# Kernel tuning notes

Hardware: AMD Instinct MI355X
Metric: run time of the kernel (lower is better)

## Reference

```python
import jax, jax.numpy as jnp
import numpy as np

B, Himg, Wimg, C, NH = 16, 64, 64, 256, 8
HD = C // NH  # 32
N = Himg * Wimg  # 4096


def _rotations(h, w, hd):
    # RMT/RAVLT 2D axial RoPE: head_dim split into two halves (rows, cols),
    # each half holds k_max = hd//4 complex frequencies.
    k_max = hd // 4
    theta = 1.0 / (10000.0 ** (np.arange(k_max) / k_max))
    ang_h = np.arange(h)[:, None] * theta  # (h, k_max)
    ang_w = np.arange(w)[:, None] * theta  # (w, k_max)
    ang = np.concatenate([
        np.broadcast_to(ang_h[:, None, :], (h, w, k_max)),
        np.broadcast_to(ang_w[None, :, :], (h, w, k_max)),
    ], axis=-1)  # (h, w, hd//2)
    return jnp.asarray(np.cos(ang), jnp.float32), jnp.asarray(np.sin(ang), jnp.float32)

COS, SIN = _rotations(Himg, Wimg, HD)


def _rope(x):
    # x: (b, nh, H, W, hd); complex rotation of (even, odd) channel pairs
    xr, xi = x[..., 0::2], x[..., 1::2]
    out_r = xr * COS - xi * SIN
    out_i = xr * SIN + xi * COS
    return jnp.stack([out_r, out_i], axis=-1).reshape(x.shape)


def setup_inputs() -> dict:
    key = jax.random.key(0)
    ks = jax.random.split(key, 5)
    return {
        "x": jax.random.normal(ks[0], (B, N, C), jnp.float32),
        "w_qkvo": jax.random.normal(ks[1], (C, 4 * C), jnp.float32) * 0.02,
        "b_qkvo": jnp.zeros((4 * C,), jnp.float32),
        "lepe_w": jax.random.normal(ks[2], (C, 1, 5, 5), jnp.float32) * 0.02,
        "lepe_b": jnp.zeros((C,), jnp.float32),
        "w_proj": jax.random.normal(ks[3], (C, C), jnp.float32) * 0.02,
        "b_proj": jnp.zeros((C,), jnp.float32),
    }


def reference(x, w_qkvo, b_qkvo, lepe_w, lepe_b, w_proj, b_proj):
    b, n, c = x.shape
    scale = HD ** -0.5
    qkvo = x @ w_qkvo + b_qkvo  # (b, n, 4c)
    q, k, v, o = (qkvo[..., i * c:(i + 1) * c] for i in range(4))
    # LePE: depthwise 5x5 conv on v viewed as an image
    v_img = v.reshape(b, Himg, Wimg, c).transpose(0, 3, 1, 2)  # NCHW
    lepe = jax.lax.conv_general_dilated(
        v_img, lepe_w, window_strides=(1, 1), padding=[(2, 2), (2, 2)],
        dimension_numbers=("NCHW", "OIHW", "NCHW"), feature_group_count=c,
    ) + lepe_b[None, :, None, None]
    # ELU+1 feature map
    q = jax.nn.elu(q) + 1.0
    k = jax.nn.elu(k) + 1.0
    q = q.reshape(b, n, NH, HD).transpose(0, 2, 1, 3)  # (b, nh, n, hd)
    k = k.reshape(b, n, NH, HD).transpose(0, 2, 1, 3)
    v = v.reshape(b, n, NH, HD).transpose(0, 2, 1, 3)
    # efficiency reweighting of keys
    q_mean = q.mean(axis=-2, keepdims=True)  # (b, nh, 1, hd)
    eff = jax.nn.softmax(scale * jnp.einsum("bhod,bhnd->bhon", q_mean, k), axis=-1)
    k = k * eff.transpose(0, 1, 3, 2) * n  # (b, nh, n, hd)
    # RoPE on q and reweighted k
    q_rope = _rope(q.reshape(b, NH, Himg, Wimg, HD)).reshape(b, NH, n, HD)
    k_rope = _rope(k.reshape(b, NH, Himg, Wimg, HD)).reshape(b, NH, n, HD)
    # normalizer from non-rope q and mean of reweighted k
    z = 1.0 / (jnp.einsum("bhnd,bhod->bhno", q, k.mean(axis=-2, keepdims=True)) + 1e-6)
    # linear attention: kv accumulation then q @ kv (scale n^-1 split as n^-0.5 each)
    inv_sqrt_n = n ** -0.5
    kv = jnp.einsum("bhnd,bhne->bhde", k_rope * inv_sqrt_n, v * inv_sqrt_n)  # (b, nh, hd, hd)
    out = jnp.einsum("bhnd,bhde->bhne", q_rope, kv) * z
    out = out.transpose(0, 2, 1, 3).reshape(b, n, c)
    out = out + lepe.transpose(0, 2, 3, 1).reshape(b, n, c)
    out = out * o  # gate
    return out @ w_proj + b_proj
```

## Files before the change

kernel.cpp:

```cpp
#include <hip/hip_runtime.h>
#include <math.h>

constexpr int B   = 16;
constexpr int IH  = 64;
constexpr int IW  = 64;
constexpr int C   = 256;
constexpr int NH  = 8;
constexpr int HD  = 32;
constexpr int N   = IH * IW;
constexpr int C4  = 4 * C;
constexpr int KVP_STRIDE = 1060;

using f16x8 = __attribute__((ext_vector_type(8))) _Float16;
using f32x4 = __attribute__((ext_vector_type(4))) float;

__global__ void k_tables(float* __restrict__ cosT, float* __restrict__ sinT) {
  int t = blockIdx.x * 256 + threadIdx.x;
  int j = t & 15, pix = t >> 4;
  int y = pix >> 6, x = pix & 63;
  int jj = j & 7;
  double theta = pow(10000.0, -(double)jj / 8.0);
  double pos = (j < 8) ? (double)y : (double)x;
  double ang = pos * theta;
  cosT[t] = (float)cos(ang);
  sinT[t] = (float)sin(ang);
}

__global__ void k_split_wT(const float* __restrict__ w, int ldb,
                           _Float16* __restrict__ hiT, _Float16* __restrict__ loT) {
  int n = blockIdx.x;
  int k = threadIdx.x;
  float v = w[(size_t)k * ldb + n];
  _Float16 h = (_Float16)v;
  hiT[(size_t)n * 256 + k] = h;
  loT[(size_t)n * 256 + k] = (_Float16)(v - (float)h);
}

__global__ __launch_bounds__(256) void k_gemm_split(
    const float* __restrict__ A, int lda,
    const _Float16* __restrict__ BhT, const _Float16* __restrict__ BlT,
    const float* __restrict__ bias, float* __restrict__ Cm, int ldc,
    int nelu, float* __restrict__ qpart) {
  __shared__ _Float16 lds[4 * 5120];
  _Float16* AhL = lds;
  _Float16* AlL = lds + 5120;
  _Float16* BhL = lds + 10240;
  _Float16* BlL = lds + 15360;
  int t = threadIdx.x;
  int m0 = blockIdx.x * 128, n0 = blockIdx.y * 128;
  int lane = t & 63;
  int wm = t >> 7, wn = (t >> 6) & 1;
  int lr = lane & 15, lg = lane >> 4;
  int srow = t >> 1, sseg = t & 1;

  f32x4 acc[4][4] = {};

  const float* aP = &A[(size_t)(m0 + srow) * lda + sseg * 16];
  const _Float16* bhP = &BhT[(size_t)(n0 + srow) * 256 + sseg * 16];
  const _Float16* blP = &BlT[(size_t)(n0 + srow) * 256 + sseg * 16];

  float4 areg[2][4];
#pragma unroll
  for (int j = 0; j < 4; ++j) areg[0][j] = *(const float4*)(aP + (j << 2));
#pragma unroll
  for (int j = 0; j < 4; ++j) areg[1][j] = *(const float4*)(aP + 32 + (j << 2));
  f16x8 brh0 = *(const f16x8*)(bhP + 0);
  f16x8 brh1 = *(const f16x8*)(bhP + 8);
  f16x8 brl0 = *(const f16x8*)(blP + 0);
  f16x8 brl1 = *(const f16x8*)(blP + 8);

#pragma unroll
  for (int it = 0; it < 8; ++it) {
    const int kc = it * 32;
    const int cur = it & 1;
    {
      float av[16];
#pragma unroll
      for (int j = 0; j < 4; ++j) {
        av[j * 4 + 0] = areg[cur][j].x; av[j * 4 + 1] = areg[cur][j].y;
        av[j * 4 + 2] = areg[cur][j].z; av[j * 4 + 3] = areg[cur][j].w;
      }
      f16x8 h0, h1, l0, l1;
#pragma unroll
      for (int j = 0; j < 8; ++j) {
        _Float16 h = (_Float16)av[j];
        h0[j] = h; l0[j] = (_Float16)(av[j] - (float)h);
        _Float16 h2 = (_Float16)av[j + 8];
        h1[j] = h2; l1[j] = (_Float16)(av[j + 8] - (float)h2);
      }
      int d = srow * 40 + sseg * 16;
      *(f16x8*)&AhL[d] = h0; *(f16x8*)&AhL[d + 8] = h1;
      *(f16x8*)&AlL[d] = l0; *(f16x8*)&AlL[d + 8] = l1;
      *(f16x8*)&BhL[d] = brh0; *(f16x8*)&BhL[d + 8] = brh1;
      *(f16x8*)&BlL[d] = brl0; *(f16x8*)&BlL[d + 8] = brl1;
    }
    __syncthreads();

    if (it < 6) {
#pragma unroll
      for (int j = 0; j < 4; ++j)
        areg[cur][j] = *(const float4*)(aP + kc + 64 + (j << 2));
    }
    if (it < 7) {
      brh0 = *(const f16x8*)(bhP + kc + 32);
      brh1 = *(const f16x8*)(bhP + kc + 40);
      brl0 = *(const f16x8*)(blP + kc + 32);
      brl1 = *(const f16x8*)(blP + kc + 40);
    }

    f16x8 ah[4], al[4];
#pragma unroll
    for (int mi = 0; mi < 4; ++mi) {
      int ar = (wm * 64 + mi * 16 + lr) * 40 + lg * 8;
      ah[mi] = *(const f16x8*)&AhL[ar];
      al[mi] = *(const f16x8*)&AlL[ar];
    }
#pragma unroll
    for (int ni = 0; ni < 4; ++ni) {
      int br = (wn * 64 + ni * 16 + lr) * 40 + lg * 8;
      f16x8 bh = *(const f16x8*)&BhL[br];
      f16x8 bl = *(const f16x8*)&BlL[br];
#pragma unroll
      for (int mi = 0; mi < 4; ++mi) {
        acc[mi][ni] = __builtin_amdgcn_mfma_f32_16x16x32_f16(ah[mi], bh, acc[mi][ni], 0, 0, 0);
        acc[mi][ni] = __builtin_amdgcn_mfma_f32_16x16x32_f16(al[mi], bh, acc[mi][ni], 0, 0, 0);
        acc[mi][ni] = __builtin_amdgcn_mfma_f32_16x16x32_f16(ah[mi], bl, acc[mi][ni], 0, 0, 0);
      }
    }
    __syncthreads();
  }

  float* Cl = reinterpret_cast<float*>(lds);
  int ri2 = t >> 3, c0 = (t & 7) << 4;
  bool doq = (qpart != nullptr) && (n0 < 256);
  float qs[16] = {};
#pragma unroll
  for (int mi = 0; mi < 4; ++mi) {
#pragma unroll
    for (int ni = 0; ni < 4; ++ni) {
      int col = wn * 64 + ni * 16 + lr;
#pragma unroll
      for (int r = 0; r < 4; ++r)
        Cl[(wm * 16 + lg * 4 + r) * 132 + col] = acc[mi][ni][r];
    }
    __syncthreads();
    int grow = m0 + (ri2 >> 4) * 64 + mi * 16 + (ri2 & 15);
#pragma unroll
    for (int j = 0; j < 4; ++j) {
      int col = n0 + c0 + j * 4;
      float4 v = *(const float4*)&Cl[ri2 * 132 + c0 + j * 4];
      float4 bb = *(const float4*)&bias[col];
      v.x += bb.x; v.y += bb.y; v.z += bb.z; v.w += bb.w;
      if (col < nelu) {
        v.x = (v.x > 0.f) ? v.x + 1.f : expf(v.x);
        v.y = (v.y > 0.f) ? v.y + 1.f : expf(v.y);
        v.z = (v.z > 0.f) ? v.z + 1.f : expf(v.z);
        v.w = (v.w > 0.f) ? v.w + 1.f : expf(v.w);
      }
      if (doq) {
        qs[j * 4 + 0] += v.x; qs[j * 4 + 1] += v.y;
        qs[j * 4 + 2] += v.z; qs[j * 4 + 3] += v.w;
      }
      *(float4*)&Cm[(size_t)grow * ldc + col] = v;
    }
    __syncthreads();
  }
  if (doq) {
#pragma unroll
    for (int j = 0; j < 4; ++j) {
      float4 w4 = {qs[j*4+0], qs[j*4+1], qs[j*4+2], qs[j*4+3]};
      *(float4*)&Cl[ri2 * 132 + c0 + j * 4] = w4;
    }
    __syncthreads();
    if (t < 128) {
      float ssum = 0.f;
#pragma unroll
      for (int rr = 0; rr < 32; ++rr) ssum += Cl[rr * 132 + t];
      int b_local = m0 >> 12, rowblk = (m0 >> 7) & 31;
      qpart[(size_t)(b_local * 32 + rowblk) * 256 + n0 + t] = ssum;
    }
  }
}

__global__ __launch_bounds__(256) void k_kvflash(
    const float* __restrict__ qkvo, const float* __restrict__ qpart,
    const float* __restrict__ cosT, const float* __restrict__ sinT,
    float* __restrict__ kvp) {
  __shared__ float qm[32];
  __shared__ float sL[512];
  __shared__ float red[256];
  __shared__ float ktG[4][32][36];
  __shared__ float vtG[4][32][36];
  int bh = blockIdx.x, chunk = blockIdx.y;
  int b = bh >> 3, h = bh & 7;
  int t = threadIdx.x;
  int nbase = chunk << 9;

  if (t < 32) {
    float s = 0.f;
#pragma unroll
    for (int rb = 0; rb < 32; ++rb)
      s += qpart[(size_t)(b * 32 + rb) * 256 + (h << 5) + t];
    qm[t] = s * (1.0f / N) * 0.1767766952966369f;
  }
  __syncthreads();

  float qmr[32];
#pragma unroll
  for (int i = 0; i < 32; ++i) qmr[i] = qm[i];
  float mx = -3.4e38f;
#pragma unroll
  for (int i = 0; i < 2; ++i) {
    int n = nbase + t + i * 256;
    const float* kp = &qkvo[(size_t)(b * N + n) * C4 + 256 + (h << 5)];
    float dot = 0.f;
#pragma unroll
    for (int j = 0; j < 8; ++j) {
      float4 k4 = *(const float4*)(kp + (j << 2));
      dot += k4.x * qmr[j*4] + k4.y * qmr[j*4+1] + k4.z * qmr[j*4+2] + k4.w * qmr[j*4+3];
    }
    sL[t + i * 256] = dot;
    mx = fmaxf(mx, dot);
  }
  red[t] = mx; __syncthreads();
  for (int off = 128; off > 0; off >>= 1) {
    if (t < off) red[t] = fmaxf(red[t], red[t + off]);
    __syncthreads();
  }
  float mx_c = red[0];
  __syncthreads();
  float psum = expf(sL[t] - mx_c) + expf(sL[t + 256] - mx_c);
  red[t] = psum; __syncthreads();
  for (int off = 128; off > 0; off >>= 1) {
    if (t < off) red[t] += red[t + off];
    __syncthreads();
  }
  float sum_c = red[0];

  int sg = t >> 6;
  int lane = t & 63;
  int d0 = (lane >> 3) << 2;
  int e0 = (lane & 7) << 2;
  int srow_l = (t >> 1) & 31;
  int sdh = t & 1;
  float acc[4][4] = {};
  float km16[16] = {};

  for (int s = 0; s < 4; ++s) {
    int nloc = sg * 128 + s * 32 + srow_l;
    int n = nbase + nloc;
    const float* kp = &qkvo[(size_t)(b * N + n) * C4 + 256 + (h << 5) + sdh * 16];
    const float* vp = kp + 256;
    float ef = expf(sL[nloc] - mx_c);
    float kl[16], vl[16];
#pragma unroll
    for (int j4 = 0; j4 < 4; ++j4) {
      float4 k4 = *(const float4*)(kp + (j4 << 2));
      float4 v4 = *(const float4*)(vp + (j4 << 2));
      k4.x *= ef; k4.y *= ef; k4.z *= ef; k4.w *= ef;
      km16[j4*4+0] += k4.x; km16[j4*4+1] += k4.y;
      km16[j4*4+2] += k4.z; km16[j4*4+3] += k4.w;
      kl[j4*4+0] = k4.x; kl[j4*4+1] = k4.y; kl[j4*4+2] = k4.z; kl[j4*4+3] = k4.w;
      vl[j4*4+0] = v4.x; vl[j4*4+1] = v4.y; vl[j4*4+2] = v4.z; vl[j4*4+3] = v4.w;
    }
#pragma unroll
    for (int p = 0; p < 8; ++p) {
      float cc = cosT[(n << 4) + sdh * 8 + p];
      float sn = sinT[(n << 4) + sdh * 8 + p];
      float kr = kl[2*p], ki = kl[2*p+1];
      kl[2*p]   = kr * cc - ki * sn;
      kl[2*p+1] = kr * sn + ki * cc;
    }
#pragma unroll
    for (int j4 = 0; j4 < 4; ++j4) {
      float4 kw = {kl[j4*4+0], kl[j4*4+1], kl[j4*4+2], kl[j4*4+3]};
      float4 vw = {vl[j4*4+0], vl[j4*4+1], vl[j4*4+2], vl[j4*4+3]};
      *(float4*)&ktG[sg][srow_l][sdh*16 + (j4 << 2)] = kw;
      *(float4*)&vtG[sg][srow_l][sdh*16 + (j4 << 2)] = vw;
    }
    __syncthreads();
    __builtin_amdgcn_s_setprio(1);
#pragma unroll
    for (int nn = 0; nn < 32; ++nn) {
      float4 k4 = *(const float4*)&ktG[sg][nn][d0];
      float4 v4 = *(const float4*)&vtG[sg][nn][e0];
      float kv_[4] = {k4.x, k4.y, k4.z, k4.w};
      float vv_[4] = {v4.x, v4.y, v4.z, v4.w};
#pragma unroll
      for (int i = 0; i < 4; ++i)
#pragma unroll
        for (int j = 0; j < 4; ++j)
          acc[i][j] = fmaf(kv_[i], vv_[j], acc[i][j]);
    }
    __builtin_amdgcn_s_setprio(0);
    __syncthreads();
  }

  float* mrg = &ktG[0][0][0];
#pragma unroll
  for (int i = 0; i < 4; ++i)
#pragma unroll
    for (int j = 0; j < 4; ++j)
      mrg[sg * 1024 + (d0 + i) * 32 + (e0 + j)] = acc[i][j];
  __syncthreads();
  size_t o = (size_t)(bh * 8 + chunk) * KVP_STRIDE;
  {
    int idx = t << 2;
    float4 r;
    r.x = mrg[idx+0] + mrg[1024+idx+0] + mrg[2048+idx+0] + mrg[3072+idx+0];
    r.y = mrg[idx+1] + mrg[1024+idx+1] + mrg[2048+idx+1] + mrg[3072+idx+1];
    r.z = mrg[idx+2] + mrg[1024+idx+2] + mrg[2048+idx+2] + mrg[3072+idx+2];
    r.w = mrg[idx+3] + mrg[1024+idx+3] + mrg[2048+idx+3] + mrg[3072+idx+3];
    kvp[o + idx + 0] = r.x; kvp[o + idx + 1] = r.y;
    kvp[o + idx + 2] = r.z; kvp[o + idx + 3] = r.w;
  }
  float* kmb = &vtG[0][0][0];
#pragma unroll
  for (int j = 0; j < 16; ++j) kmb[t * 16 + j] = km16[j];
  __syncthreads();
  if (t < 32) {
    int dh = t >> 4, dj = t & 15;
    float ssum = 0.f;
    for (int r = 0; r < 128; ++r) ssum += kmb[((r << 1) + dh) * 16 + dj];
    kvp[o + 1024 + t] = ssum;
  }
  if (t == 0) {
    kvp[o + 1056] = mx_c;
    kvp[o + 1057] = sum_c;
  }
}

__global__ __launch_bounds__(256) void k_lepe(
    const float* __restrict__ qkvo, const float* __restrict__ wgt,
    const float* __restrict__ lb, float* __restrict__ lepe_out, int b0) {
  int blk = blockIdx.x;
  int b = blk >> 8, rem = blk & 255;
  int y = rem >> 2, x0 = (rem & 3) << 4;
  int c = threadIdx.x;
  float w[25];
#pragma unroll
  for (int i = 0; i < 25; ++i) w[i] = wgt[c * 25 + i];
  float bias = lb[c];
  float acc[16];
#pragma unroll
  for (int p = 0; p < 16; ++p) acc[p] = bias;
#pragma unroll
  for (int dy = 0; dy < 5; ++dy) {
    int yy = y + dy - 2;
    if (yy < 0 || yy >= IH) continue;
    size_t rowb = (size_t)(b * N + (yy << 6)) * C4 + 512 + c;
#pragma unroll
    for (int dx = 0; dx < 5; ++dx) {
      float wv = w[dy * 5 + dx];
#pragma unroll
      for (int p = 0; p < 16; ++p) {
        int xx = x0 + p + dx - 2;
        if (xx < 0 || xx >= IW) continue;
        acc[p] = fmaf(qkvo[rowb + (size_t)xx * C4], wv, acc[p]);
      }
    }
  }
#pragma unroll
  for (int p = 0; p < 16; ++p)
    lepe_out[(size_t)((b0 + b) * N + (y << 6) + x0 + p) * C + c] = acc[p];
}

__global__ __launch_bounds__(256) void k_out_combine(
    float* __restrict__ qkvo, const float* __restrict__ kvp,
    const float* __restrict__ cosT, const float* __restrict__ sinT,
    const float* __restrict__ lepe, int b0) {
  __shared__ float kvs[1024];
  __shared__ float kms[32];
  __shared__ float fcs[8];
  int bh = blockIdx.x, chunk = blockIdx.y;
  int b = bh >> 3, h = bh & 7;
  int t = threadIdx.x;
  if (t == 0) {
    float mxs[8], sums[8];
    float mx = -3.4e38f;
#pragma unroll
    for (int c = 0; c < 8; ++c) {
      size_t o = (size_t)(bh * 8 + c) * KVP_STRIDE;
      mxs[c] = kvp[o + 1056];
      sums[c] = kvp[o + 1057];
      mx = fmaxf(mx, mxs[c]);
    }
    float T = 0.f;
#pragma unroll
    for (int c = 0; c < 8; ++c) T += sums[c] * expf(mxs[c] - mx);
    float invT = 1.0f / T;
#pragma unroll
    for (int c = 0; c < 8; ++c) fcs[c] = expf(mxs[c] - mx) * invT;
  }
  __syncthreads();
  {
    int idx = t << 2;
    size_t o0 = (size_t)(bh * 8) * KVP_STRIDE + idx;
    float4 r = {0.f, 0.f, 0.f, 0.f};
#pragma unroll
    for (int c = 0; c < 8; ++c) {
      float4 p = *(const float4*)&kvp[o0 + (size_t)c * KVP_STRIDE];
      float f = fcs[c];
      r.x += p.x * f; r.y += p.y * f; r.z += p.z * f; r.w += p.w * f;
    }
    *(float4*)&kvs[idx] = r;
    if (t < 32) {
      float s = 0.f;
#pragma unroll
      for (int c = 0; c < 8; ++c)
        s += kvp[(size_t)(bh * 8 + c) * KVP_STRIDE + 1024 + t] * fcs[c];
      kms[t] = s;
    }
  }
  __syncthreads();
  int n = (chunk << 8) + t;
  size_t rowbase = (size_t)(b * N + n) * C4;
  float q[32];
#pragma unroll
  for (int i = 0; i < 8; ++i) {
    float4 q4 = *reinterpret_cast<const float4*>(&qkvo[rowbase + (h << 5) + (i << 2)]);
    q[i * 4 + 0] = q4.x; q[i * 4 + 1] = q4.y; q[i * 4 + 2] = q4.z; q[i * 4 + 3] = q4.w;
  }
  float dot = 0.f;
#pragma unroll
  for (int dd = 0; dd < 32; ++dd) dot += q[dd] * kms[dd];
  float zv = 1.0f / (dot + 1e-6f);
  const float* cp = &cosT[n << 4];
  const float* sp = &sinT[n << 4];
#pragma unroll
  for (int j = 0; j < 16; ++j) {
    float cc = cp[j], ss = sp[j];
    float qr = q[2 * j], qi = q[2 * j + 1];
    q[2 * j]     = qr * cc - qi * ss;
    q[2 * j + 1] = qr * ss + qi * cc;
  }
  size_t oc = (size_t)((b0 + b) * N + n) * C + (h << 5);
#pragma unroll
  for (int e4 = 0; e4 < 8; ++e4) {
    float ax = 0, ay = 0, az = 0, aw = 0;
#pragma unroll
    for (int dd = 0; dd < 32; ++dd) {
      float4 kv4 = *reinterpret_cast<const float4*>(&kvs[(dd << 5) + (e4 << 2)]);
      float qd = q[dd];
      ax = fmaf(qd, kv4.x, ax); ay = fmaf(qd, kv4.y, ay);
      az = fmaf(qd, kv4.z, az); aw = fmaf(qd, kv4.w, aw);
    }
    float4 lp = *reinterpret_cast<const float4*>(&lepe[oc + (e4 << 2)]);
    float4 ov = *reinterpret_cast<const float4*>(
        &qkvo[rowbase + 768 + (h << 5) + (e4 << 2)]);
    float4 r;
    r.x = (ax * zv + lp.x) * ov.x;
    r.y = (ay * zv + lp.y) * ov.y;
    r.z = (az * zv + lp.z) * ov.z;
    r.w = (aw * zv + lp.w) * ov.w;
    *reinterpret_cast<float4*>(&qkvo[rowbase + (h << 5) + (e4 << 2)]) = r;
  }
}

static inline size_t ws_bytes_needed(int bpp) {
  size_t pn = (size_t)bpp * N;
  size_t f32c = pn * C4
              + (size_t)bpp * 32 * 256
              + (size_t)bpp * NH * 8 * KVP_STRIDE
              + (size_t)N * 16 * 2;
  size_t f16c = (size_t)C * C4 * 2
              + (size_t)C * C * 2;
  return f32c * 4 + f16c * 2;
}

extern "C" void kernel_launch(void* const* d_in, const int* in_sizes, int n_in,
                              void* d_out, int out_size, void* d_ws, size_t ws_size,
                              hipStream_t stream) {
  const float* x      = (const float*)d_in[0];
  const float* w_qkvo = (const float*)d_in[1];
  const float* b_qkvo = (const float*)d_in[2];
  const float* lepe_w = (const float*)d_in[3];
  const float* lepe_b = (const float*)d_in[4];
  const float* w_proj = (const float*)d_in[5];
  const float* b_proj = (const float*)d_in[6];
  float* out = (float*)d_out;
  float* ws  = (float*)d_ws;

  int bpp = 2;
  if (ws_bytes_needed(16) <= ws_size) bpp = 16;
  else if (ws_bytes_needed(8) <= ws_size) bpp = 8;
  else if (ws_bytes_needed(4) <= ws_size) bpp = 4;

  size_t pn = (size_t)bpp * N;
  int nbh = bpp * NH;
  float* qkvo  = ws;
  float* qpart = qkvo  + pn * C4;
  float* kvp   = qpart + (size_t)bpp * 32 * 256;
  float* cosT  = kvp   + (size_t)nbh * 8 * KVP_STRIDE;
  float* sinT  = cosT  + (size_t)N * 16;
  _Float16* wqh = (_Float16*)(sinT + (size_t)N * 16);
  _Float16* wql = wqh + (size_t)C * C4;
  _Float16* wph = wql + (size_t)C * C4;
  _Float16* wpl = wph + (size_t)C * C;

  k_tables<<<N * 16 / 256, 256, 0, stream>>>(cosT, sinT);
  k_split_wT<<<C4, 256, 0, stream>>>(w_qkvo, C4, wqh, wql);
  k_split_wT<<<C, 256, 0, stream>>>(w_proj, C, wph, wpl);

  for (int b0 = 0; b0 < B; b0 += bpp) {
    k_gemm_split<<<dim3(pn / 128, C4 / 128), 256, 0, stream>>>(
        x + (size_t)b0 * N * C, C, wqh, wql, b_qkvo, qkvo, C4, 512, qpart);
    k_kvflash<<<dim3(nbh, 8), 256, 0, stream>>>(qkvo, qpart, cosT, sinT, kvp);
    k_lepe<<<bpp * IH * 4, 256, 0, stream>>>(qkvo, lepe_w, lepe_b, out, b0);
    k_out_combine<<<dim3(nbh, 16), 256, 0, stream>>>(qkvo, kvp, cosT, sinT, out, b0);
    k_gemm_split<<<dim3(pn / 128, C / 128), 256, 0, stream>>>(
        qkvo, C4, wph, wpl, b_proj, out + (size_t)b0 * N * C, C, 0, nullptr);
  }
}
```

Before: 550.3 us.

## Merge prologue kernels, fuse LePE into kvflash launch, simplify GEMM prefetch

Merges the table-building and weight-splitting kernels into one prologue launch, and puts the LePE conv blocks into the same grid as the kv accumulation kernel so the two independent stages run side by side. The GEMM main loop changes from a two-deep register prefetch of A to a single-stage prefetch in a non-unrolled loop. This cuts launch count and may improve overlap. The shallower prefetch and the dropped unroll may expose more global-load latency in the dominant GEMM, and the shared kernel's larger LDS footprint now applies to the LePE blocks too.

```diff
diff --git a/kernel.cpp b/kernel.cpp
--- a/kernel.cpp
+++ b/kernel.cpp
@@ -14,26 +14,36 @@
 using f16x8 = __attribute__((ext_vector_type(8))) _Float16;
 using f32x4 = __attribute__((ext_vector_type(4))) float;
 
-__global__ void k_tables(float* __restrict__ cosT, float* __restrict__ sinT) {
-  int t = blockIdx.x * 256 + threadIdx.x;
-  int j = t & 15, pix = t >> 4;
-  int y = pix >> 6, x = pix & 63;
-  int jj = j & 7;
-  double theta = pow(10000.0, -(double)jj / 8.0);
-  double pos = (j < 8) ? (double)y : (double)x;
-  double ang = pos * theta;
-  cosT[t] = (float)cos(ang);
-  sinT[t] = (float)sin(ang);
-}
-
-__global__ void k_split_wT(const float* __restrict__ w, int ldb,
-                           _Float16* __restrict__ hiT, _Float16* __restrict__ loT) {
-  int n = blockIdx.x;
-  int k = threadIdx.x;
-  float v = w[(size_t)k * ldb + n];
-  _Float16 h = (_Float16)v;
-  hiT[(size_t)n * 256 + k] = h;
-  loT[(size_t)n * 256 + k] = (_Float16)(v - (float)h);
+__global__ void k_prologue(const float* __restrict__ w_qkvo,
+                           const float* __restrict__ w_proj,
+                           float* __restrict__ cosT, float* __restrict__ sinT,
+                           _Float16* __restrict__ wqh, _Float16* __restrict__ wql,
+                           _Float16* __restrict__ wph, _Float16* __restrict__ wpl) {
+  int bid = blockIdx.x;
+  int tid = threadIdx.x;
+  if (bid < 256) {
+    int t = bid * 256 + tid;
+    int j = t & 15, pix = t >> 4;
+    int y = pix >> 6, x = pix & 63;
+    int jj = j & 7;
+    double theta = pow(10000.0, -(double)jj / 8.0);
+    double pos = (j < 8) ? (double)y : (double)x;
+    double ang = pos * theta;
+    cosT[t] = (float)cos(ang);
+    sinT[t] = (float)sin(ang);
+  } else if (bid < 256 + C4) {
+    int n = bid - 256;
+    float v = w_qkvo[(size_t)tid * C4 + n];
+    _Float16 h = (_Float16)v;
+    wqh[(size_t)n * 256 + tid] = h;
+    wql[(size_t)n * 256 + tid] = (_Float16)(v - (float)h);
+  } else {
+    int n = bid - 256 - C4;
+    float v = w_proj[(size_t)tid * C + n];
+    _Float16 h = (_Float16)v;
+    wph[(size_t)n * 256 + tid] = h;
+    wpl[(size_t)n * 256 + tid] = (_Float16)(v - (float)h);
+  }
 }
 
 __global__ __launch_bounds__(256) void k_gemm_split(
@@ -58,28 +68,19 @@
   const float* aP = &A[(size_t)(m0 + srow) * lda + sseg * 16];
   const _Float16* bhP = &BhT[(size_t)(n0 + srow) * 256 + sseg * 16];
   const _Float16* blP = &BlT[(size_t)(n0 + srow) * 256 + sseg * 16];
-
-  float4 areg[2][4];
-#pragma unroll
-  for (int j = 0; j < 4; ++j) areg[0][j] = *(const float4*)(aP + (j << 2));
-#pragma unroll
-  for (int j = 0; j < 4; ++j) areg[1][j] = *(const float4*)(aP + 32 + (j << 2));
+  float4 ar0 = *(const float4*)(aP + 0);
+  float4 ar1 = *(const float4*)(aP + 4);
+  float4 ar2 = *(const float4*)(aP + 8);
+  float4 ar3 = *(const float4*)(aP + 12);
   f16x8 brh0 = *(const f16x8*)(bhP + 0);
   f16x8 brh1 = *(const f16x8*)(bhP + 8);
   f16x8 brl0 = *(const f16x8*)(blP + 0);
   f16x8 brl1 = *(const f16x8*)(blP + 8);
 
-#pragma unroll
-  for (int it = 0; it < 8; ++it) {
-    const int kc = it * 32;
-    const int cur = it & 1;
+  for (int kc = 0; kc < 256; kc += 32) {
     {
-      float av[16];
-#pragma unroll
-      for (int j = 0; j < 4; ++j) {
-        av[j * 4 + 0] = areg[cur][j].x; av[j * 4 + 1] = areg[cur][j].y;
-        av[j * 4 + 2] = areg[cur][j].z; av[j * 4 + 3] = areg[cur][j].w;
-      }
+      float av[16] = {ar0.x, ar0.y, ar0.z, ar0.w, ar1.x, ar1.y, ar1.z, ar1.w,
+                      ar2.x, ar2.y, ar2.z, ar2.w, ar3.x, ar3.y, ar3.z, ar3.w};
       f16x8 h0, h1, l0, l1;
 #pragma unroll
       for (int j = 0; j < 8; ++j) {
@@ -96,16 +97,18 @@
     }
     __syncthreads();
 
-    if (it < 6) {
-#pragma unroll
-      for (int j = 0; j < 4; ++j)
-        areg[cur][j] = *(const float4*)(aP + kc + 64 + (j << 2));
-    }
-    if (it < 7) {
-      brh0 = *(const f16x8*)(bhP + kc + 32);
-      brh1 = *(const f16x8*)(bhP + kc + 40);
-      brl0 = *(const f16x8*)(blP + kc + 32);
-      brl1 = *(const f16x8*)(blP + kc + 40);
+    if (kc + 32 < 256) {
+      const float* aN = aP + kc + 32;
+      const _Float16* bhN = bhP + kc + 32;
+      const _Float16* blN = blP + kc + 32;
+      ar0 = *(const float4*)(aN + 0);
+      ar1 = *(const float4*)(aN + 4);
+      ar2 = *(const float4*)(aN + 8);
+      ar3 = *(const float4*)(aN + 12);
+      brh0 = *(const f16x8*)(bhN + 0);
+      brh1 = *(const f16x8*)(bhN + 8);
+      brl0 = *(const f16x8*)(blN + 0);
+      brl1 = *(const f16x8*)(blN + 8);
     }
 
     f16x8 ah[4], al[4];
@@ -182,18 +185,56 @@
   }
 }
 
-__global__ __launch_bounds__(256) void k_kvflash(
+__global__ __launch_bounds__(256) void k_kvflash_lepe(
     const float* __restrict__ qkvo, const float* __restrict__ qpart,
     const float* __restrict__ cosT, const float* __restrict__ sinT,
-    float* __restrict__ kvp) {
+    float* __restrict__ kvp,
+    const float* __restrict__ lepe_w, const float* __restrict__ lepe_b,
+    float* __restrict__ lepe_out, int b0, int kvN) {
   __shared__ float qm[32];
   __shared__ float sL[512];
   __shared__ float red[256];
   __shared__ float ktG[4][32][36];
   __shared__ float vtG[4][32][36];
-  int bh = blockIdx.x, chunk = blockIdx.y;
+  int bid = blockIdx.x;
+  int t = threadIdx.x;
+
+  if (bid >= kvN) {
+    int blk = bid - kvN;
+    int b = blk >> 8, rem = blk & 255;
+    int y = rem >> 2, x0 = (rem & 3) << 4;
+    int c = t;
+    float w[25];
+#pragma unroll
+    for (int i = 0; i < 25; ++i) w[i] = lepe_w[c * 25 + i];
+    float bias = lepe_b[c];
+    float acc[16];
+#pragma unroll
+    for (int p = 0; p < 16; ++p) acc[p] = bias;
+#pragma unroll
+    for (int dy = 0; dy < 5; ++dy) {
+      int yy = y + dy - 2;
+      if (yy < 0 || yy >= IH) continue;
+      size_t rowb = (size_t)(b * N + (yy << 6)) * C4 + 512 + c;
+#pragma unroll
+      for (int dx = 0; dx < 5; ++dx) {
+        float wv = w[dy * 5 + dx];
+#pragma unroll
+        for (int p = 0; p < 16; ++p) {
+          int xx = x0 + p + dx - 2;
+          if (xx < 0 || xx >= IW) continue;
+          acc[p] = fmaf(qkvo[rowb + (size_t)xx * C4], wv, acc[p]);
+        }
+      }
+    }
+#pragma unroll
+    for (int p = 0; p < 16; ++p)
+      lepe_out[(size_t)((b0 + b) * N + (y << 6) + x0 + p) * C + c] = acc[p];
+    return;
+  }
+
+  int bh = bid >> 3, chunk = bid & 7;
   int b = bh >> 3, h = bh & 7;
-  int t = threadIdx.x;
   int nbase = chunk << 9;
 
   if (t < 32) {
@@ -330,41 +371,6 @@
   }
 }
 
-__global__ __launch_bounds__(256) void k_lepe(
-    const float* __restrict__ qkvo, const float* __restrict__ wgt,
-    const float* __restrict__ lb, float* __restrict__ lepe_out, int b0) {
-  int blk = blockIdx.x;
-  int b = blk >> 8, rem = blk & 255;
-  int y = rem >> 2, x0 = (rem & 3) << 4;
-  int c = threadIdx.x;
-  float w[25];
-#pragma unroll
-  for (int i = 0; i < 25; ++i) w[i] = wgt[c * 25 + i];
-  float bias = lb[c];
-  float acc[16];
-#pragma unroll
-  for (int p = 0; p < 16; ++p) acc[p] = bias;
-#pragma unroll
-  for (int dy = 0; dy < 5; ++dy) {
-    int yy = y + dy - 2;
-    if (yy < 0 || yy >= IH) continue;
-    size_t rowb = (size_t)(b * N + (yy << 6)) * C4 + 512 + c;
-#pragma unroll
-    for (int dx = 0; dx < 5; ++dx) {
-      float wv = w[dy * 5 + dx];
-#pragma unroll
-      for (int p = 0; p < 16; ++p) {
-        int xx = x0 + p + dx - 2;
-        if (xx < 0 || xx >= IW) continue;
-        acc[p] = fmaf(qkvo[rowb + (size_t)xx * C4], wv, acc[p]);
-      }
-    }
-  }
-#pragma unroll
-  for (int p = 0; p < 16; ++p)
-    lepe_out[(size_t)((b0 + b) * N + (y << 6) + x0 + p) * C + c] = acc[p];
-}
-
 __global__ __launch_bounds__(256) void k_out_combine(
     float* __restrict__ qkvo, const float* __restrict__ kvp,
     const float* __restrict__ cosT, const float* __restrict__ sinT,
@@ -498,15 +504,15 @@
   _Float16* wph = wql + (size_t)C * C4;
   _Float16* wpl = wph + (size_t)C * C;
 
-  k_tables<<<N * 16 / 256, 256, 0, stream>>>(cosT, sinT);
-  k_split_wT<<<C4, 256, 0, stream>>>(w_qkvo, C4, wqh, wql);
-  k_split_wT<<<C, 256, 0, stream>>>(w_proj, C, wph, wpl);
+  k_prologue<<<256 + C4 + C, 256, 0, stream>>>(w_qkvo, w_proj, cosT, sinT,
+                                               wqh, wql, wph, wpl);
 
   for (int b0 = 0; b0 < B; b0 += bpp) {
     k_gemm_split<<<dim3(pn / 128, C4 / 128), 256, 0, stream>>>(
         x + (size_t)b0 * N * C, C, wqh, wql, b_qkvo, qkvo, C4, 512, qpart);
-    k_kvflash<<<dim3(nbh, 8), 256, 0, stream>>>(qkvo, qpart, cosT, sinT, kvp);
-    k_lepe<<<bpp * IH * 4, 256, 0, stream>>>(qkvo, lepe_w, lepe_b, out, b0);
+    int kvN = nbh * 8;
+    k_kvflash_lepe<<<kvN + bpp * 256, 256, 0, stream>>>(
+        qkvo, qpart, cosT, sinT, kvp, lepe_w, lepe_b, out, b0, kvN);
     k_out_combine<<<dim3(nbh, 16), 256, 0, stream>>>(qkvo, kvp, cosT, sinT, out, b0);
     k_gemm_split<<<dim3(pn / 128, C / 128), 256, 0, stream>>>(
         qkvo, C4, wph, wpl, b_proj, out + (size_t)b0 * N * C, C, 0, nullptr);
```

Measured after the change: 507.5 us. 1.08x faster.
